# Kernel optimization log

Hardware: AMD Instinct MI355X
Metric: run time of the kernel (lower is better)

Reference implementation:

```python
import jax, jax.numpy as jnp
import numpy as np

B, T, N, L, D, F = 8, 1024, 512, 4096, 512, 64  # batch, target, nodes, leaves, d_model, d_feature
BR = L // N  # branching factor: leaves per node


def setup_inputs() -> dict:
    key = jax.random.key(0)
    ks = jax.random.split(key, 10)
    s = 0.02
    return {
        "root": jax.random.normal(ks[0], (B, 1, F), dtype=jnp.float32),
        "node": jax.random.normal(ks[1], (B, N, D), dtype=jnp.float32),
        "leaf": jax.random.normal(ks[2], (B, L, D), dtype=jnp.float32),
        "target": jax.random.normal(ks[3], (B, T, D), dtype=jnp.float32),
        "Wq": jax.random.normal(ks[4], (D, F), dtype=jnp.float32) * s,
        "bq": jnp.zeros((F,), dtype=jnp.float32),
        "Wk": jax.random.normal(ks[5], (D, F), dtype=jnp.float32) * s,
        "bk": jnp.zeros((F,), dtype=jnp.float32),
        "Wv": jax.random.normal(ks[6], (D, F), dtype=jnp.float32) * s,
        "bv": jnp.zeros((F,), dtype=jnp.float32),
        "Wagg": jax.random.normal(ks[7], (D, 1), dtype=jnp.float32) * s,
        "bagg": jnp.zeros((1,), dtype=jnp.float32),
    }


def reference(root, node, leaf, target, Wq, bq, Wk, bk, Wv, bv, Wagg, bagg):
    # Shared DecoderLinear projections (same weights used for node and leaf).
    q = target @ Wq + bq                      # [B,T,F]
    node_k = node @ Wk + bk                   # [B,N,F]
    node_v = node @ Wv + bv                   # [B,N,F]
    leaf_k = leaf @ Wk + bk                   # [B,L,F]
    leaf_v = leaf @ Wv + bv                   # [B,L,F]

    scale = 1.0 / jnp.sqrt(jnp.asarray(F, dtype=q.dtype))
    # Dual-key attention weights (no value-matmul inside attention()).
    Aqn = jax.nn.softmax(jnp.einsum('btf,bnf->btn', q, node_k) * scale, axis=-1)  # [B,T,N]
    Aql = jax.nn.softmax(jnp.einsum('btf,blf->btl', q, leaf_k) * scale, axis=-1)  # [B,T,L]

    # Tree interpolation: each leaf mixes root, its parent node value, and itself.
    node_rep = jnp.repeat(node_v, BR, axis=1)               # [B,L,F]
    interp = (root + node_rep + leaf_v) / 3.0               # [B,L,F]

    # Upward cumulative aggregation: suffix mean along the leaf dimension.
    rev_cumsum = jnp.cumsum(interp[:, ::-1, :], axis=1)[:, ::-1, :]  # [B,L,F]
    counts = (L - jnp.arange(L)).astype(interp.dtype)[None, :, None]
    upward = rev_cumsum / counts                                     # [B,L,F]

    # Weighted aggregation: learned softmax weights over each node's leaf group.
    w = jax.nn.softmax((leaf @ Wagg + bagg).reshape(B, N, BR), axis=-1)   # [B,N,BR]
    node_hat = jnp.einsum('bnc,bncf->bnf', w, upward.reshape(B, N, BR, F))  # [B,N,F]

    # Fused cat + matmul + softmax.
    A = jnp.concatenate([Aqn, Aql], axis=-1)          # [B,T,N+L]
    V = jnp.concatenate([node_hat, leaf_v], axis=-2)  # [B,N+L,F]
    return jax.nn.softmax(jnp.einsum('btm,bmf->btf', A, V), axis=-1)  # [B,T,F]
```

## Files before the change

kernel.cpp:

```cpp
#include <hip/hip_runtime.h>

#define B_ 8
#define T_ 1024
#define N_ 512
#define L_ 4096
#define D_ 512
#define F_ 64
#define SLICES 8
#define TPS 9
#define KSTR 72
#define XSTR 264

typedef __attribute__((ext_vector_type(8))) short short8;
typedef __attribute__((ext_vector_type(4))) float f32x4;

__device__ __forceinline__ unsigned short f2bf(float x){
    unsigned u = __builtin_bit_cast(unsigned, x);
    u += 0x7FFFu + ((u >> 16) & 1u);
    return (unsigned short)(u >> 16);
}
__device__ __forceinline__ unsigned pack_bf(float lo, float hi){
    return (unsigned)f2bf(lo) | ((unsigned)f2bf(hi) << 16);
}
__device__ __forceinline__ float bf2f(unsigned short s){
    return __builtin_bit_cast(float, ((unsigned)s) << 16);
}
__device__ __forceinline__ short8 frag_from4(unsigned d0, unsigned d1, unsigned d2, unsigned d3){
    union { unsigned u[4]; short8 s; } t;
    t.u[0] = d0; t.u[1] = d1; t.u[2] = d2; t.u[3] = d3;
    return t.s;
}

__global__ __launch_bounds__(64)
void prep_kernel(const float* __restrict__ Wq, const float* __restrict__ bq,
                 const float* __restrict__ Wk, const float* __restrict__ bk,
                 const float* __restrict__ Wv, const float* __restrict__ bv,
                 unsigned short* __restrict__ Wq_t, unsigned short* __restrict__ Wkv_t,
                 float* __restrict__ bq_s, float* __restrict__ bkv)
{
    const int n = blockIdx.x;
    const int lane = threadIdx.x;
    if (n == 192) {
        bq_s[lane]   = bq[lane] * 0.125f;
        bkv[lane]    = bk[lane];
        bkv[64+lane] = bv[lane];
        return;
    }
    const int d0 = lane * 8;
    unsigned short t[8];
    if (n < 64) {
        #pragma unroll
        for (int j = 0; j < 8; ++j) t[j] = f2bf(Wq[(size_t)(d0+j)*F_ + n] * 0.125f);
        *(uint4*)&Wq_t[(size_t)n*D_ + d0] = make_uint4(
            (unsigned)t[0]|((unsigned)t[1]<<16), (unsigned)t[2]|((unsigned)t[3]<<16),
            (unsigned)t[4]|((unsigned)t[5]<<16), (unsigned)t[6]|((unsigned)t[7]<<16));
    } else {
        const int nn  = n - 64;
        const float* W = (nn < 64) ? Wk : Wv;
        const int col = nn & 63;
        #pragma unroll
        for (int j = 0; j < 8; ++j) t[j] = f2bf(W[(size_t)(d0+j)*F_ + col]);
        *(uint4*)&Wkv_t[(size_t)nn*D_ + d0] = make_uint4(
            (unsigned)t[0]|((unsigned)t[1]<<16), (unsigned)t[2]|((unsigned)t[3]<<16),
            (unsigned)t[4]|((unsigned)t[5]<<16), (unsigned)t[6]|((unsigned)t[7]<<16));
    }
}

template<int MODE>
__device__ __forceinline__ void proj_body(
    int r0, unsigned short* Xs, unsigned short* Ws, unsigned short* Vt_lds,
    const float* __restrict__ X,
    const unsigned short* __restrict__ Wt,
    const float* __restrict__ bias,
    const float* __restrict__ Wagg, const float* __restrict__ bagg,
    unsigned short* __restrict__ outK, float* __restrict__ outVf,
    unsigned short* __restrict__ outVt, float* __restrict__ outAgg)
{
    constexpr int NPASS = (MODE == 0) ? 1 : 2;
    const int tid = threadIdx.x;
    const int l = tid & 63, c = l & 15, h = l >> 4;
    const int w  = tid >> 6;
    const int nt = w & 3;
    const int m  = w >> 2;
    const int wr = tid >> 4, wch = tid & 15;

    float4 xr0[4], xr1[4];
    #pragma unroll
    for (int j = 0; j < 4; ++j) {
        const int s = tid + j*1024, row = s >> 6, col = s & 63;
        xr0[j] = *(const float4*)(X + (size_t)(r0+row)*D_ + col*4);
    }
    #pragma unroll
    for (int j = 0; j < 4; ++j) {
        const int s = tid + j*1024, row = s >> 6, col = s & 63;
        xr1[j] = *(const float4*)(X + (size_t)(r0+row)*D_ + 256 + col*4);
    }
    uint4 wreg[2];
    #pragma unroll
    for (int j = 0; j < 2; ++j)
        wreg[j] = *(const uint4*)(Wt + (size_t)wr*D_ + (wch + j*16)*8);

    f32x4 acc0 = {0,0,0,0};
    f32x4 acc1 = {0,0,0,0};
    float pa = 0.f;

    auto writeX = [&](const float4* xr) {
        #pragma unroll
        for (int j = 0; j < 4; ++j) {
            const int s = tid + j*1024, row = s >> 6, col = s & 63;
            *(uint2*)&Xs[row*XSTR + col*4] =
                make_uint2(pack_bf(xr[j].x, xr[j].y), pack_bf(xr[j].z, xr[j].w));
        }
    };
    auto writeW = [&]() {
        #pragma unroll
        for (int j = 0; j < 2; ++j)
            *(uint4*)&Ws[wr*XSTR + (wch + j*16)*8] = wreg[j];
    };
    auto issueW = [&](int p, int kc) {
        #pragma unroll
        for (int j = 0; j < 2; ++j)
            wreg[j] = *(const uint4*)(Wt + (size_t)(64*p + wr)*D_ + kc*256 + (wch + j*16)*8);
    };
    auto compute = [&](f32x4& acc) {
        #pragma unroll
        for (int kk = 0; kk < 8; ++kk) {
            const short8 bfr = *(const short8*)&Ws[(16*nt + c)*XSTR + kk*32 + 8*h];
            const short8 af  = *(const short8*)&Xs[(16*m  + c)*XSTR + kk*32 + 8*h];
            acc = __builtin_amdgcn_mfma_f32_16x16x32_bf16(af, bfr, acc, 0,0,0);
        }
    };
    auto aggpart = [&](int kc) {
        const int row = tid >> 4, qd = tid & 15;
        const unsigned short* xr = &Xs[row*XSTR + qd*16];
        const float* wrg = Wagg + kc*256 + qd*16;
        #pragma unroll
        for (int j = 0; j < 2; ++j) {
            const short8 xv = *(const short8*)(xr + j*8);
            const float4 wa0 = *(const float4*)(wrg + j*8);
            const float4 wa1 = *(const float4*)(wrg + j*8 + 4);
            pa += bf2f((unsigned short)xv[0])*wa0.x + bf2f((unsigned short)xv[1])*wa0.y
                + bf2f((unsigned short)xv[2])*wa0.z + bf2f((unsigned short)xv[3])*wa0.w
                + bf2f((unsigned short)xv[4])*wa1.x + bf2f((unsigned short)xv[5])*wa1.y
                + bf2f((unsigned short)xv[6])*wa1.z + bf2f((unsigned short)xv[7])*wa1.w;
        }
    };

    writeX(xr0);
    writeW();
    __syncthreads();
    if constexpr (NPASS == 2) {
        issueW(1, 0);
        compute(acc0);
        __syncthreads();
        writeW();
        __syncthreads();
        issueW(0, 1);
        compute(acc1);
        if constexpr (MODE == 2) aggpart(0);
        __syncthreads();
    } else {
        issueW(0, 1);
        compute(acc0);
        __syncthreads();
    }
    writeX(xr1);
    writeW();
    __syncthreads();
    if constexpr (NPASS == 2) {
        issueW(1, 1);
        compute(acc0);
        __syncthreads();
        writeW();
        __syncthreads();
        compute(acc1);
        if constexpr (MODE == 2) aggpart(1);
    } else {
        compute(acc0);
    }

    {
        const float bc0 = bias[16*nt + c];
        #pragma unroll
        for (int r = 0; r < 4; ++r) {
            const int row = r0 + 16*m + 4*h + r;
            outK[(size_t)row*F_ + 16*nt + c] = f2bf(acc0[r] + bc0);
        }
    }
    if constexpr (NPASS == 2) {
        const float bc1 = bias[64 + 16*nt + c];
        #pragma unroll
        for (int r = 0; r < 4; ++r) {
            const int row = r0 + 16*m + 4*h + r;
            const float v = acc1[r] + bc1;
            if constexpr (MODE == 1) {
                outVf[(size_t)row*F_ + 16*nt + c] = v;
            } else {
                Vt_lds[(16*nt + c)*72 + 16*m + 4*h + r] = f2bf(v);
            }
        }
    }

    if constexpr (MODE == 2) {
        {
            const int row = tid >> 4, qd = tid & 15;
            pa += __shfl_xor(pa, 1);
            pa += __shfl_xor(pa, 2);
            pa += __shfl_xor(pa, 4);
            pa += __shfl_xor(pa, 8);
            if (qd == 0) outAgg[r0 + row] = pa + bagg[0];
        }
        __syncthreads();
        {
            const int f = tid >> 4, seg = tid & 15;
            const int b = r0 >> 12, l0 = r0 & (L_ - 1);
            const uint2 a0 = *(const uint2*)&Vt_lds[f*72 + seg*4];
            *(uint2*)(outVt + ((size_t)(b*F_ + f))*L_ + l0 + seg*4) = a0;
        }
    }
}

__global__ __launch_bounds__(1024, 8)
void proj_all(const float* __restrict__ target, const float* __restrict__ node,
              const float* __restrict__ leaf,
              const unsigned short* __restrict__ Wq_t,
              const unsigned short* __restrict__ Wkv_t,
              const float* __restrict__ bq_s, const float* __restrict__ bkv,
              const float* __restrict__ Wagg, const float* __restrict__ bagg,
              unsigned short* __restrict__ q_bf, unsigned short* __restrict__ nk_bf,
              float* __restrict__ node_v, unsigned short* __restrict__ lk_bf,
              unsigned short* __restrict__ lvt, float* __restrict__ agg)
{
    __shared__ unsigned short Xs[64 * XSTR];
    __shared__ unsigned short Ws[64 * XSTR];
    __shared__ unsigned short Vt_lds[64 * 72];
    const int blk = blockIdx.x;
    if (blk < 512) {
        proj_body<2>(blk*64, Xs, Ws, Vt_lds, leaf, Wkv_t, bkv, Wagg, bagg,
                     lk_bf, nullptr, lvt, agg);
    } else if (blk < 640) {
        proj_body<0>((blk-512)*64, Xs, Ws, Vt_lds, target, Wq_t, bq_s, nullptr, nullptr,
                     q_bf, nullptr, nullptr, nullptr);
    } else {
        proj_body<1>((blk-640)*64, Xs, Ws, Vt_lds, node, Wkv_t, bkv, nullptr, nullptr,
                     nk_bf, node_v, nullptr, nullptr);
    }
}

__global__ __launch_bounds__(256)
void scan_nh_kernel(const unsigned short* __restrict__ lvt,
                    const float* __restrict__ node_v,
                    const float* __restrict__ root,
                    const float* __restrict__ agg,
                    unsigned short* __restrict__ nh_t)
{
    const int gtid = blockIdx.x * 256 + threadIdx.x;
    const int wv   = gtid >> 6;
    const int lane = threadIdx.x & 63;
    const int b = wv >> 6;
    const int f = wv & 63;

    const unsigned short* vt = lvt + ((size_t)(b*F_ + f))*L_ + lane*64;
    const float rootf = root[b*F_ + f];
    short8 xv[8]; float nv[8]; float gv[8];
    #pragma unroll
    for (int g = 0; g < 8; ++g) {
        xv[g] = *(const short8*)(vt + g*8);
        nv[g] = node_v[((size_t)(b*N_ + lane*8 + g))*F_ + f];
        float s8 = 0.f;
        #pragma unroll
        for (int j = 0; j < 8; ++j) s8 += bf2f((unsigned short)xv[g][j]);
        gv[g] = (s8 + 8.f*(rootf + nv[g])) * (1.f/3.f);
    }

    float s[9];
    s[8] = 0.f;
    #pragma unroll
    for (int j = 7; j >= 0; --j) s[j] = s[j+1] + gv[j];

    float x = s[0];
    const float lsum = x;
    #pragma unroll
    for (int off = 1; off < 64; off <<= 1) {
        float t = __shfl_down(x, off);
        if (lane + off < 64) x += t;
    }
    const float excl = x - lsum;

    const float* aggb = agg + (size_t)b*L_ + lane*64;
    unsigned short out8[8];
    #pragma unroll
    for (int g = 0; g < 8; ++g) {
        const float4 a0 = *(const float4*)(aggb + g*8);
        const float4 a1 = *(const float4*)(aggb + g*8 + 4);
        const float av[8] = {a0.x,a0.y,a0.z,a0.w, a1.x,a1.y,a1.z,a1.w};
        float mx = av[0];
        #pragma unroll
        for (int cc = 1; cc < 8; ++cc) mx = fmaxf(mx, av[cc]);
        float wgt[8]; float wsum = 0.f;
        #pragma unroll
        for (int cc = 0; cc < 8; ++cc) { wgt[cc] = __expf(av[cc] - mx); wsum += wgt[cc]; }

        const float tn = excl + s[g+1];
        float run = 0.f, acc = 0.f;
        #pragma unroll
        for (int cc = 7; cc >= 0; --cc) {
            const int ll = lane*64 + g*8 + cc;
            const float interp = (rootf + nv[g] + bf2f((unsigned short)xv[g][cc])) * (1.f/3.f);
            run += interp;
            const float up = (tn + run) / (float)(L_ - ll);
            acc = fmaf(wgt[cc], up, acc);
        }
        out8[g] = f2bf(acc / wsum);
    }
    *(uint4*)&nh_t[((size_t)(b*F_ + f))*N_ + lane*8] = *(const uint4*)out8;
}

__global__ __launch_bounds__(512, 4)
void attn_kernel(const unsigned short* __restrict__ qb,
                 const unsigned short* __restrict__ nk,
                 const unsigned short* __restrict__ nht,
                 const unsigned short* __restrict__ lk,
                 const unsigned short* __restrict__ lvt,
                 unsigned short* __restrict__ pacc, float* __restrict__ pd)
{
    __shared__ unsigned short Ks[2][64*KSTR];
    __shared__ unsigned short Vt[2][64*KSTR];

    const int wg  = (blockIdx.x & 7) * 64 + (blockIdx.x >> 3);
    const int b   = wg >> 6;
    const int sl  = (wg >> 3) & 7;
    const int t0  = (wg & 7) * 128;

    const int tid = threadIdx.x;
    const int w   = tid >> 6;
    const int l   = tid & 63;
    const int c   = l & 15;
    const int h   = l >> 4;
    const int sm  = tid >> 3;
    const int sc  = tid & 7;

    const unsigned short* qrow = qb + ((size_t)(b*T_ + t0 + w*16 + c))*F_ + 8*h;
    const short8 qf0 = *(const short8*)qrow;
    const short8 qf1 = *(const short8*)(qrow + 32);

    f32x4 accN[4] = {{0,0,0,0},{0,0,0,0},{0,0,0,0},{0,0,0,0}};
    f32x4 accL[4] = {{0,0,0,0},{0,0,0,0},{0,0,0,0},{0,0,0,0}};
    float dsN = 0.f, dsL = 0.f;

    const unsigned short* Knb = nk  + (size_t)b*N_*F_;
    const unsigned short* Klb = lk  + (size_t)b*L_*F_;
    const unsigned short* Vnb = nht + (size_t)b*F_*N_;
    const unsigned short* Vlb = lvt + (size_t)b*F_*L_;

    const int ti0 = sl * TPS;

    uint4 sk0, sv0;
    auto load_tile = [&](int ti) {
        if (ti < 8) {
            sk0 = *(const uint4*)(Knb + (size_t)ti*64*F_ + sm*64 + sc*8);
            sv0 = *(const uint4*)(Vnb + (size_t)sm*N_ + ti*64 + sc*8);
        } else {
            sk0 = *(const uint4*)(Klb + (size_t)(ti-8)*64*F_ + sm*64 + sc*8);
            sv0 = *(const uint4*)(Vlb + (size_t)sm*L_ + (ti-8)*64 + sc*8);
        }
    };
    auto write_tile = [&](int pb) {
        *(uint4*)&Ks[pb][sm*KSTR + sc*8] = sk0;
        *(uint4*)&Vt[pb][sm*KSTR + sc*8] = sv0;
    };

    load_tile(ti0);
    write_tile(0);
    __syncthreads();

    const int srcA = c + 16*((2*h) & 3);
    const int srcB = c + 16*((2*h + 1) & 3);
    const int hs   = h >> 1;

    for (int i = 0; i < TPS; ++i) {
        const int  ti  = ti0 + i;
        const bool isN = ti < 8;
        const int  pb  = i & 1;
        const bool nxt = (i + 1 < TPS);
        if (nxt) load_tile(ti + 1);

        f32x4 st[4] = {{0,0,0,0},{0,0,0,0},{0,0,0,0},{0,0,0,0}};
        #pragma unroll
        for (int ss = 0; ss < 4; ++ss) {
            const short8 kf0 = *(const short8*)&Ks[pb][(16*ss + c)*KSTR + 8*h];
            st[ss] = __builtin_amdgcn_mfma_f32_16x16x32_bf16(kf0, qf0, st[ss], 0,0,0);
            const short8 kf1 = *(const short8*)&Ks[pb][(16*ss + c)*KSTR + 32 + 8*h];
            st[ss] = __builtin_amdgcn_mfma_f32_16x16x32_bf16(kf1, qf1, st[ss], 0,0,0);
        }

        unsigned pk0[4], pk1[4];
        float psum = 0.f;
        #pragma unroll
        for (int ss = 0; ss < 4; ++ss) {
            #pragma unroll
            for (int r = 0; r < 4; ++r) { st[ss][r] = __expf(st[ss][r]); psum += st[ss][r]; }
            pk0[ss] = pack_bf(st[ss][0], st[ss][1]);
            pk1[ss] = pack_bf(st[ss][2], st[ss][3]);
        }
        if (isN) dsN += psum; else dsL += psum;

        #pragma unroll
        for (int k00 = 0; k00 < 2; ++k00) {
            const unsigned d0a = __shfl(pk0[2*k00+0], srcA);
            const unsigned d0b = __shfl(pk0[2*k00+1], srcA);
            const unsigned d1a = __shfl(pk1[2*k00+0], srcA);
            const unsigned d1b = __shfl(pk1[2*k00+1], srcA);
            const unsigned d2a = __shfl(pk0[2*k00+0], srcB);
            const unsigned d2b = __shfl(pk0[2*k00+1], srcB);
            const unsigned d3a = __shfl(pk1[2*k00+0], srcB);
            const unsigned d3b = __shfl(pk1[2*k00+1], srcB);
            const short8 bp = frag_from4(hs ? d0b : d0a, hs ? d1b : d1a,
                                         hs ? d2b : d2a, hs ? d3b : d3a);
            if (isN) {
                #pragma unroll
                for (int s2 = 0; s2 < 4; ++s2) {
                    const short8 af = *(const short8*)&Vt[pb][(16*s2 + c)*KSTR + 32*k00 + 8*h];
                    accN[s2] = __builtin_amdgcn_mfma_f32_16x16x32_bf16(af, bp, accN[s2], 0,0,0);
                }
            } else {
                #pragma unroll
                for (int s2 = 0; s2 < 4; ++s2) {
                    const short8 af = *(const short8*)&Vt[pb][(16*s2 + c)*KSTR + 32*k00 + 8*h];
                    accL[s2] = __builtin_amdgcn_mfma_f32_16x16x32_bf16(af, bp, accL[s2], 0,0,0);
                }
            }
        }

        if (nxt) {
            write_tile(pb ^ 1);
            __syncthreads();
        }
    }

    dsN += __shfl_xor(dsN, 16);  dsN += __shfl_xor(dsN, 32);
    dsL += __shfl_xor(dsL, 16);  dsL += __shfl_xor(dsL, 32);

    const int gt = b*T_ + t0 + w*16 + c;
    unsigned short* baseN = pacc + (((size_t)sl*(B_*T_) + gt)*2 + 0)*F_;
    unsigned short* baseL = baseN + F_;
    #pragma unroll
    for (int s2 = 0; s2 < 4; ++s2) {
        *(unsigned*)&baseN[s2*16 + 4*h]     = pack_bf(accN[s2][0], accN[s2][1]);
        *(unsigned*)&baseN[s2*16 + 4*h + 2] = pack_bf(accN[s2][2], accN[s2][3]);
        *(unsigned*)&baseL[s2*16 + 4*h]     = pack_bf(accL[s2][0], accL[s2][1]);
        *(unsigned*)&baseL[s2*16 + 4*h + 2] = pack_bf(accL[s2][2], accL[s2][3]);
    }
    if (h == 0) {
        pd[((size_t)sl*(B_*T_) + gt)*2 + 0] = dsN;
        pd[((size_t)sl*(B_*T_) + gt)*2 + 1] = dsL;
    }
}

__global__ __launch_bounds__(256)
void combine_kernel(const unsigned short* __restrict__ pacc,
                    const float* __restrict__ pd,
                    float* __restrict__ out)
{
    const int gt = (blockIdx.x * 256 + threadIdx.x) >> 6;
    const int f  = threadIdx.x & 63;

    float aN = 0.f, aL = 0.f, dN = 0.f, dL = 0.f;
    #pragma unroll
    for (int s = 0; s < SLICES; ++s) {
        const size_t base = ((size_t)s*(B_*T_) + gt)*2;
        aN += bf2f(pacc[(base + 0)*F_ + f]);
        aL += bf2f(pacc[(base + 1)*F_ + f]);
        dN += pd[base + 0];
        dL += pd[base + 1];
    }
    float lg = aN / dN + aL / dL;
    float mx = lg;
    #pragma unroll
    for (int off = 1; off < 64; off <<= 1) mx = fmaxf(mx, __shfl_xor(mx, off));
    const float e = __expf(lg - mx);
    float ssum = e;
    #pragma unroll
    for (int off = 1; off < 64; off <<= 1) ssum += __shfl_xor(ssum, off);
    out[(size_t)gt*F_ + f] = e / ssum;
}

extern "C" void kernel_launch(void* const* d_in, const int* in_sizes, int n_in,
                              void* d_out, int out_size, void* d_ws, size_t ws_size,
                              hipStream_t stream)
{
    const float* root   = (const float*)d_in[0];
    const float* node   = (const float*)d_in[1];
    const float* leaf   = (const float*)d_in[2];
    const float* target = (const float*)d_in[3];
    const float* Wq   = (const float*)d_in[4];
    const float* bq   = (const float*)d_in[5];
    const float* Wk   = (const float*)d_in[6];
    const float* bk   = (const float*)d_in[7];
    const float* Wv   = (const float*)d_in[8];
    const float* bv   = (const float*)d_in[9];
    const float* Wagg = (const float*)d_in[10];
    const float* bagg = (const float*)d_in[11];
    float* out = (float*)d_out;

    char* wp = (char*)d_ws;
    unsigned short* q_bf  = (unsigned short*)wp; wp += (size_t)B_*T_*F_*2;
    unsigned short* nk_bf = (unsigned short*)wp; wp += (size_t)B_*N_*F_*2;
    unsigned short* lk_bf = (unsigned short*)wp; wp += (size_t)B_*L_*F_*2;
    unsigned short* lvt   = (unsigned short*)wp; wp += (size_t)B_*F_*L_*2;
    unsigned short* nht   = (unsigned short*)wp; wp += (size_t)B_*F_*N_*2;
    unsigned short* Wq_t  = (unsigned short*)wp; wp += (size_t)64*D_*2;
    unsigned short* Wkv_t = (unsigned short*)wp; wp += (size_t)128*D_*2;
    float* node_v = (float*)wp; wp += (size_t)B_*N_*F_*4;
    float* agg    = (float*)wp; wp += (size_t)B_*L_*4;
    float* bq_s   = (float*)wp; wp += 512;
    float* bkv    = (float*)wp; wp += 512;
    unsigned short* pacc = (unsigned short*)wp; wp += (size_t)SLICES*B_*T_*2*F_*2;
    float* pd     = (float*)wp;

    prep_kernel<<<193, 64, 0, stream>>>(Wq, bq, Wk, bk, Wv, bv, Wq_t, Wkv_t, bq_s, bkv);
    proj_all<<<704, 1024, 0, stream>>>(target, node, leaf, Wq_t, Wkv_t, bq_s, bkv,
                                       Wagg, bagg, q_bf, nk_bf, node_v, lk_bf, lvt, agg);
    scan_nh_kernel<<<128, 256, 0, stream>>>(lvt, node_v, root, agg, nht);
    attn_kernel<<<B_*(T_/128)*SLICES, 512, 0, stream>>>(q_bf, nk_bf, nht, lk_bf, lvt, pacc, pd);
    combine_kernel<<<(B_*T_)/4, 256, 0, stream>>>(pacc, pd, out);
}
```

Before: 94.70 us.

## Halve projection block size and give each wave two N-tiles sharing A fragments

The projection kernel now runs with 512 threads instead of 1024. Each wave computes two 16-wide output column tiles that reuse one A-fragment LDS read, and the second half of X is loaded just in time instead of being held in registers from the start. The aggregation and transposed-V write paths are remapped to the new thread count with wider stores. This cuts LDS traffic per MFMA and register pressure, but leaves fewer waves per block to hide the latency of the global loads.

```diff
diff --git a/kernel.cpp b/kernel.cpp
--- a/kernel.cpp
+++ b/kernel.cpp
@@ -80,62 +80,63 @@
     const int tid = threadIdx.x;
     const int l = tid & 63, c = l & 15, h = l >> 4;
     const int w  = tid >> 6;
-    const int nt = w & 3;
-    const int m  = w >> 2;
-    const int wr = tid >> 4, wch = tid & 15;
-
-    float4 xr0[4], xr1[4];
-    #pragma unroll
-    for (int j = 0; j < 4; ++j) {
-        const int s = tid + j*1024, row = s >> 6, col = s & 63;
-        xr0[j] = *(const float4*)(X + (size_t)(r0+row)*D_ + col*4);
-    }
-    #pragma unroll
-    for (int j = 0; j < 4; ++j) {
-        const int s = tid + j*1024, row = s >> 6, col = s & 63;
-        xr1[j] = *(const float4*)(X + (size_t)(r0+row)*D_ + 256 + col*4);
-    }
-    uint4 wreg[2];
-    #pragma unroll
-    for (int j = 0; j < 2; ++j)
-        wreg[j] = *(const uint4*)(Wt + (size_t)wr*D_ + (wch + j*16)*8);
-
-    f32x4 acc0 = {0,0,0,0};
-    f32x4 acc1 = {0,0,0,0};
+    const int m  = w & 3;
+    const int nh = w >> 2;
+    const int nt0 = 2*nh, nt1 = 2*nh + 1;
+
+    float4 xreg[8];
+    uint4  wreg[4];
+
+    auto issueX = [&](int kc) {
+        #pragma unroll
+        for (int j = 0; j < 8; ++j) {
+            const int s = tid + j*512, row = s >> 6, col = s & 63;
+            xreg[j] = *(const float4*)(X + (size_t)(r0+row)*D_ + kc*256 + col*4);
+        }
+    };
+    auto writeX = [&]() {
+        #pragma unroll
+        for (int j = 0; j < 8; ++j) {
+            const int s = tid + j*512, row = s >> 6, col = s & 63;
+            *(uint2*)&Xs[row*XSTR + col*4] =
+                make_uint2(pack_bf(xreg[j].x, xreg[j].y), pack_bf(xreg[j].z, xreg[j].w));
+        }
+    };
+    auto issueW = [&](int p, int kc) {
+        #pragma unroll
+        for (int j = 0; j < 4; ++j) {
+            const int s = tid + j*512, row = s >> 5, ch = s & 31;
+            wreg[j] = *(const uint4*)(Wt + (size_t)(64*p + row)*D_ + kc*256 + ch*8);
+        }
+    };
+    auto writeW = [&]() {
+        #pragma unroll
+        for (int j = 0; j < 4; ++j) {
+            const int s = tid + j*512, row = s >> 5, ch = s & 31;
+            *(uint4*)&Ws[row*XSTR + ch*8] = wreg[j];
+        }
+    };
+
+    f32x4 aK0 = {0,0,0,0}, aK1 = {0,0,0,0};
+    f32x4 aV0 = {0,0,0,0}, aV1 = {0,0,0,0};
     float pa = 0.f;
 
-    auto writeX = [&](const float4* xr) {
+    auto compute = [&](f32x4& a0, f32x4& a1) {
+        #pragma unroll
+        for (int kk = 0; kk < 8; ++kk) {
+            const short8 af = *(const short8*)&Xs[(16*m   + c)*XSTR + kk*32 + 8*h];
+            const short8 b0 = *(const short8*)&Ws[(16*nt0 + c)*XSTR + kk*32 + 8*h];
+            const short8 b1 = *(const short8*)&Ws[(16*nt1 + c)*XSTR + kk*32 + 8*h];
+            a0 = __builtin_amdgcn_mfma_f32_16x16x32_bf16(af, b0, a0, 0,0,0);
+            a1 = __builtin_amdgcn_mfma_f32_16x16x32_bf16(af, b1, a1, 0,0,0);
+        }
+    };
+    auto aggpart = [&](int kc) {
+        const int row = tid >> 3, qd = tid & 7;
+        const unsigned short* xr = &Xs[row*XSTR + qd*32];
+        const float* wrg = Wagg + kc*256 + qd*32;
         #pragma unroll
         for (int j = 0; j < 4; ++j) {
-            const int s = tid + j*1024, row = s >> 6, col = s & 63;
-            *(uint2*)&Xs[row*XSTR + col*4] =
-                make_uint2(pack_bf(xr[j].x, xr[j].y), pack_bf(xr[j].z, xr[j].w));
-        }
-    };
-    auto writeW = [&]() {
-        #pragma unroll
-        for (int j = 0; j < 2; ++j)
-            *(uint4*)&Ws[wr*XSTR + (wch + j*16)*8] = wreg[j];
-    };
-    auto issueW = [&](int p, int kc) {
-        #pragma unroll
-        for (int j = 0; j < 2; ++j)
-            wreg[j] = *(const uint4*)(Wt + (size_t)(64*p + wr)*D_ + kc*256 + (wch + j*16)*8);
-    };
-    auto compute = [&](f32x4& acc) {
-        #pragma unroll
-        for (int kk = 0; kk < 8; ++kk) {
-            const short8 bfr = *(const short8*)&Ws[(16*nt + c)*XSTR + kk*32 + 8*h];
-            const short8 af  = *(const short8*)&Xs[(16*m  + c)*XSTR + kk*32 + 8*h];
-            acc = __builtin_amdgcn_mfma_f32_16x16x32_bf16(af, bfr, acc, 0,0,0);
-        }
-    };
-    auto aggpart = [&](int kc) {
-        const int row = tid >> 4, qd = tid & 15;
-        const unsigned short* xr = &Xs[row*XSTR + qd*16];
-        const float* wrg = Wagg + kc*256 + qd*16;
-        #pragma unroll
-        for (int j = 0; j < 2; ++j) {
             const short8 xv = *(const short8*)(xr + j*8);
             const float4 wa0 = *(const float4*)(wrg + j*8);
             const float4 wa1 = *(const float4*)(wrg + j*8 + 4);
@@ -146,81 +147,91 @@
         }
     };
 
-    writeX(xr0);
+    issueX(0);
+    issueW(0, 0);
+    writeX();
     writeW();
     __syncthreads();
+
     if constexpr (NPASS == 2) {
         issueW(1, 0);
-        compute(acc0);
+        compute(aK0, aK1);
         __syncthreads();
         writeW();
         __syncthreads();
+        issueX(1);
         issueW(0, 1);
-        compute(acc1);
+        compute(aV0, aV1);
         if constexpr (MODE == 2) aggpart(0);
         __syncthreads();
-    } else {
-        issueW(0, 1);
-        compute(acc0);
-        __syncthreads();
-    }
-    writeX(xr1);
-    writeW();
-    __syncthreads();
-    if constexpr (NPASS == 2) {
+        writeX();
+        writeW();
+        __syncthreads();
         issueW(1, 1);
-        compute(acc0);
+        compute(aK0, aK1);
         __syncthreads();
         writeW();
         __syncthreads();
-        compute(acc1);
+        compute(aV0, aV1);
         if constexpr (MODE == 2) aggpart(1);
     } else {
-        compute(acc0);
+        issueX(1);
+        issueW(0, 1);
+        compute(aK0, aK1);
+        __syncthreads();
+        writeX();
+        writeW();
+        __syncthreads();
+        compute(aK0, aK1);
     }
 
     {
-        const float bc0 = bias[16*nt + c];
+        const float b0 = bias[16*nt0 + c];
+        const float b1 = bias[16*nt1 + c];
         #pragma unroll
         for (int r = 0; r < 4; ++r) {
             const int row = r0 + 16*m + 4*h + r;
-            outK[(size_t)row*F_ + 16*nt + c] = f2bf(acc0[r] + bc0);
+            outK[(size_t)row*F_ + 16*nt0 + c] = f2bf(aK0[r] + b0);
+            outK[(size_t)row*F_ + 16*nt1 + c] = f2bf(aK1[r] + b1);
         }
     }
     if constexpr (NPASS == 2) {
-        const float bc1 = bias[64 + 16*nt + c];
+        const float b0 = bias[64 + 16*nt0 + c];
+        const float b1 = bias[64 + 16*nt1 + c];
         #pragma unroll
         for (int r = 0; r < 4; ++r) {
             const int row = r0 + 16*m + 4*h + r;
-            const float v = acc1[r] + bc1;
+            const float v0 = aV0[r] + b0;
+            const float v1 = aV1[r] + b1;
             if constexpr (MODE == 1) {
-                outVf[(size_t)row*F_ + 16*nt + c] = v;
+                outVf[(size_t)row*F_ + 16*nt0 + c] = v0;
+                outVf[(size_t)row*F_ + 16*nt1 + c] = v1;
             } else {
-                Vt_lds[(16*nt + c)*72 + 16*m + 4*h + r] = f2bf(v);
+                Vt_lds[(16*nt0 + c)*72 + 16*m + 4*h + r] = f2bf(v0);
+                Vt_lds[(16*nt1 + c)*72 + 16*m + 4*h + r] = f2bf(v1);
             }
         }
     }
 
     if constexpr (MODE == 2) {
         {
-            const int row = tid >> 4, qd = tid & 15;
+            const int row = tid >> 3, qd = tid & 7;
             pa += __shfl_xor(pa, 1);
             pa += __shfl_xor(pa, 2);
             pa += __shfl_xor(pa, 4);
-            pa += __shfl_xor(pa, 8);
             if (qd == 0) outAgg[r0 + row] = pa + bagg[0];
         }
         __syncthreads();
         {
-            const int f = tid >> 4, seg = tid & 15;
+            const int f = tid >> 3, seg = tid & 7;
             const int b = r0 >> 12, l0 = r0 & (L_ - 1);
-            const uint2 a0 = *(const uint2*)&Vt_lds[f*72 + seg*4];
-            *(uint2*)(outVt + ((size_t)(b*F_ + f))*L_ + l0 + seg*4) = a0;
-        }
-    }
-}
-
-__global__ __launch_bounds__(1024, 8)
+            const uint4 a0 = *(const uint4*)&Vt_lds[f*72 + seg*8];
+            *(uint4*)(outVt + ((size_t)(b*F_ + f))*L_ + l0 + seg*8) = a0;
+        }
+    }
+}
+
+__global__ __launch_bounds__(512, 4)
 void proj_all(const float* __restrict__ target, const float* __restrict__ node,
               const float* __restrict__ leaf,
               const unsigned short* __restrict__ Wq_t,
@@ -519,8 +530,8 @@
     float* pd     = (float*)wp;
 
     prep_kernel<<<193, 64, 0, stream>>>(Wq, bq, Wk, bk, Wv, bv, Wq_t, Wkv_t, bq_s, bkv);
-    proj_all<<<704, 1024, 0, stream>>>(target, node, leaf, Wq_t, Wkv_t, bq_s, bkv,
-                                       Wagg, bagg, q_bf, nk_bf, node_v, lk_bf, lvt, agg);
+    proj_all<<<704, 512, 0, stream>>>(target, node, leaf, Wq_t, Wkv_t, bq_s, bkv,
+                                      Wagg, bagg, q_bf, nk_bf, node_v, lk_bf, lvt, agg);
     scan_nh_kernel<<<128, 256, 0, stream>>>(lvt, node_v, root, agg, nht);
     attn_kernel<<<B_*(T_/128)*SLICES, 512, 0, stream>>>(q_bf, nk_bf, nht, lk_bf, lvt, pacc, pd);
     combine_kernel<<<(B_*T_)/4, 256, 0, stream>>>(pacc, pd, out);
```

Result: slower. 117.3 us (+23.9%).
